# Kernel optimization log

Hardware: AMD Instinct MI355X
Metric: run time of the kernel (lower is better)

## Reference

```python
import jax, jax.numpy as jnp
import numpy as np

NUM_SEGMENTS = 50000


def _mlp(x, W1, b1, W2, b2):
    # hidden layer with ReLU, linear output (num_hidden_lyr=1)
    h = jax.nn.relu(x @ W1 + b1)
    return h @ W2 + b2


def setup_inputs() -> dict:
    key = jax.random.key(0)
    ks = jax.random.split(key, 10)
    N, D = 1000000, 128
    ins = jax.random.normal(ks[0], (N, D), dtype=jnp.float32)
    batch = jnp.sort(jax.random.randint(ks[1], (N,), 0, NUM_SEGMENTS, dtype=jnp.int64))
    s = 1.0 / np.sqrt(D)
    phi_W1 = jax.random.uniform(ks[2], (D, D), jnp.float32, -s, s)
    phi_b1 = jax.random.uniform(ks[3], (D,), jnp.float32, -s, s)
    phi_W2 = jax.random.uniform(ks[4], (D, D), jnp.float32, -s, s)
    phi_b2 = jax.random.uniform(ks[5], (D,), jnp.float32, -s, s)
    rho_W1 = jax.random.uniform(ks[6], (D, D), jnp.float32, -s, s)
    rho_b1 = jax.random.uniform(ks[7], (D,), jnp.float32, -s, s)
    rho_W2 = jax.random.uniform(ks[8], (D, D), jnp.float32, -s, s)
    rho_b2 = jax.random.uniform(ks[9], (D,), jnp.float32, -s, s)
    return {"ins": ins, "batch": batch, "dim": 0,
            "phi_W1": phi_W1, "phi_b1": phi_b1, "phi_W2": phi_W2, "phi_b2": phi_b2,
            "rho_W1": rho_W1, "rho_b1": rho_b1, "rho_W2": rho_W2, "rho_b2": rho_b2}


def reference(ins, batch, dim, phi_W1, phi_b1, phi_W2, phi_b2, rho_W1, rho_b1, rho_W2, rho_b2):
    # dim is always 0 in this usage (scatter over set elements)
    h = _mlp(ins, phi_W1, phi_b1, phi_W2, phi_b2)          # [N, out_dim]
    seg_sum = jax.ops.segment_sum(h, batch, num_segments=NUM_SEGMENTS)  # [B, out_dim]
    counts = jax.ops.segment_sum(jnp.ones((h.shape[0],), h.dtype), batch,
                                 num_segments=NUM_SEGMENTS)
    seg_mean = seg_sum / jnp.maximum(counts, 1.0)[:, None]  # scatter_mean semantics
    return _mlp(seg_mean, rho_W1, rho_b1, rho_W2, rho_b2)   # [B, out_dim]
```

## Files before the change

### kernel.cpp

```cpp
#include <hip/hip_runtime.h>
#include <hip/hip_fp16.h>

typedef _Float16 f16;
typedef __attribute__((ext_vector_type(8))) _Float16 f16x8;
typedef __attribute__((ext_vector_type(4))) _Float16 f16x4;
typedef __attribute__((ext_vector_type(4))) float f32x4;

#define NSEG 50000
#define DIM 128
#define LDST 136

#define MFMA16(a, b, c) __builtin_amdgcn_mfma_f32_16x16x32_f16((a), (b), (c), 0, 0, 0)

__global__ void zero2_kernel(float4* __restrict__ a, int n4a,
                             float4* __restrict__ b, int n4b) {
    int i = blockIdx.x * blockDim.x + threadIdx.x;
    float4 z = make_float4(0.f, 0.f, 0.f, 0.f);
    if (i < n4a) {
        a[i] = z;
    } else {
        int j = i - n4a;
        if (j < n4b) b[j] = z;
    }
}

__global__ void prepack_kernel(const float* __restrict__ w0, const float* __restrict__ w1,
                               const float* __restrict__ w2, const float* __restrict__ w3,
                               f16* __restrict__ packs) {
    int gid = blockIdx.x * blockDim.x + threadIdx.x;
    int q = gid >> 11;
    int r = gid & 2047;
    int tm = r >> 8;
    int kt = (r >> 6) & 3;
    int lane = r & 63;
    const float* W = (q == 0) ? w0 : (q == 1) ? w1 : (q == 2) ? w2 : w3;
    int mp = tm * 16 + (lane & 15);
    int kb = kt * 32 + ((lane >> 4) & 3) * 8;
    f16* dst = packs + q * 16384 + ((size_t)((tm * 4 + kt) * 64 + lane)) * 8;
#pragma unroll
    for (int j = 0; j < 8; ++j)
        dst[j] = (f16)W[(size_t)(kb + j) * DIM + mp];
}

__global__ __launch_bounds__(256, 4)
void phi_scatter_kernel(const float* __restrict__ x, const int* __restrict__ batch,
                        const f16* __restrict__ pack1, const f16* __restrict__ pack2,
                        const float* __restrict__ b1, const float* __restrict__ b2,
                        float* __restrict__ seg_sum, float* __restrict__ counts, int N) {
    __shared__ f16 buf[128 * LDST];
    __shared__ int seg_s[128];

    int tid = threadIdx.x;
    int wave = tid >> 6, lane = tid & 63, g = lane >> 4, ln = lane & 15;
    long long r0 = (long long)blockIdx.x * 128;
    int nvalid = min(128, N - (int)r0);

#pragma unroll
    for (int i = 0; i < 16; ++i) {
        int flat = i * 1024 + tid * 4;
        int row = flat >> 7, col = flat & 127;
        float4 v = make_float4(0.f, 0.f, 0.f, 0.f);
        if (row < nvalid) v = *(const float4*)(x + (r0 + row) * DIM + col);
        f16x4 h;
        h[0] = (f16)v.x; h[1] = (f16)v.y; h[2] = (f16)v.z; h[3] = (f16)v.w;
        *(f16x4*)(buf + row * LDST + col) = h;
    }
    if (tid < 128) {
        int s = 0;
        if (tid < nvalid) {
            s = batch[r0 + tid];
            s = (s < 0) ? 0 : ((s >= NSEG) ? NSEG - 1 : s);
        } else {
            s = -1;
        }
        seg_s[tid] = s;
    }
    __syncthreads();

    int tm0 = wave * 2;
    f32x4 acc[2][8];
#pragma unroll
    for (int a = 0; a < 2; ++a)
#pragma unroll
        for (int t = 0; t < 8; ++t) acc[a][t] = (f32x4){0.f, 0.f, 0.f, 0.f};

#pragma unroll
    for (int kt = 0; kt < 4; ++kt) {
        f16x8 a0 = *(const f16x8*)(pack1 + ((size_t)((tm0 + 0) * 4 + kt) * 64 + lane) * 8);
        f16x8 a1 = *(const f16x8*)(pack1 + ((size_t)((tm0 + 1) * 4 + kt) * 64 + lane) * 8);
#pragma unroll
        for (int tn = 0; tn < 8; ++tn) {
            f16x8 b = *(const f16x8*)(buf + (tn * 16 + ln) * LDST + kt * 32 + g * 8);
            acc[0][tn] = MFMA16(a0, b, acc[0][tn]);
            acc[1][tn] = MFMA16(a1, b, acc[1][tn]);
        }
    }
    __syncthreads();

#pragma unroll
    for (int a = 0; a < 2; ++a) {
        int tm = tm0 + a;
        float4 bv = *(const float4*)(b1 + tm * 16 + g * 4);
#pragma unroll
        for (int tn = 0; tn < 8; ++tn) {
            f32x4 c = acc[a][tn];
            f16x4 h;
            h[0] = (f16)fmaxf(c[0] + bv.x, 0.f);
            h[1] = (f16)fmaxf(c[1] + bv.y, 0.f);
            h[2] = (f16)fmaxf(c[2] + bv.z, 0.f);
            h[3] = (f16)fmaxf(c[3] + bv.w, 0.f);
            *(f16x4*)(buf + (tn * 16 + ln) * LDST + tm * 16 + g * 4) = h;
        }
    }
    __syncthreads();

#pragma unroll
    for (int a = 0; a < 2; ++a)
#pragma unroll
        for (int t = 0; t < 8; ++t) acc[a][t] = (f32x4){0.f, 0.f, 0.f, 0.f};
#pragma unroll
    for (int kt = 0; kt < 4; ++kt) {
        f16x8 a0 = *(const f16x8*)(pack2 + ((size_t)((tm0 + 0) * 4 + kt) * 64 + lane) * 8);
        f16x8 a1 = *(const f16x8*)(pack2 + ((size_t)((tm0 + 1) * 4 + kt) * 64 + lane) * 8);
#pragma unroll
        for (int tn = 0; tn < 8; ++tn) {
            f16x8 b = *(const f16x8*)(buf + (tn * 16 + ln) * LDST + kt * 32 + g * 8);
            acc[0][tn] = MFMA16(a0, b, acc[0][tn]);
            acc[1][tn] = MFMA16(a1, b, acc[1][tn]);
        }
    }
    __syncthreads();

#pragma unroll
    for (int a = 0; a < 2; ++a) {
        int tm = tm0 + a;
        float4 bv = *(const float4*)(b2 + tm * 16 + g * 4);
#pragma unroll
        for (int tn = 0; tn < 8; ++tn) {
            f32x4 c = acc[a][tn];
            f16x4 h;
            h[0] = (f16)(c[0] + bv.x);
            h[1] = (f16)(c[1] + bv.y);
            h[2] = (f16)(c[2] + bv.z);
            h[3] = (f16)(c[3] + bv.w);
            *(f16x4*)(buf + (tn * 16 + ln) * LDST + tm * 16 + g * 4) = h;
        }
    }
    __syncthreads();

    int n = tid & 127, half = tid >> 7;
    int m0 = half * 64;
    float accv = 0.f, cnt = 0.f;
    int cur = seg_s[m0];
#pragma unroll
    for (int grp = 0; grp < 8; ++grp) {
        float v[8];
        int s[8];
#pragma unroll
        for (int j = 0; j < 8; ++j) {
            int m = m0 + grp * 8 + j;
            s[j] = seg_s[m];
            v[j] = (float)buf[m * LDST + n];
        }
#pragma unroll
        for (int j = 0; j < 8; ++j) {
            if (s[j] != cur) {
                if (cur >= 0) {
                    atomicAdd(seg_sum + (size_t)cur * DIM + n, accv);
                    if (n == 0) atomicAdd(counts + cur, cnt);
                }
                accv = 0.f; cnt = 0.f; cur = s[j];
            }
            accv += v[j]; cnt += 1.f;
        }
    }
    if (cur >= 0) {
        atomicAdd(seg_sum + (size_t)cur * DIM + n, accv);
        if (n == 0) atomicAdd(counts + cur, cnt);
    }
}

#define RROWS 64
__global__ __launch_bounds__(256, 4)
void rho_kernel(const float* __restrict__ seg_sum, const float* __restrict__ counts,
                const f16* __restrict__ pack1, const f16* __restrict__ pack2,
                const float* __restrict__ b1, const float* __restrict__ b2,
                float* __restrict__ out) {
    __shared__ f16 buf[RROWS * LDST];

    int tid = threadIdx.x;
    int wave = tid >> 6, lane = tid & 63, g = lane >> 4, ln = lane & 15;
    int s0 = blockIdx.x * RROWS;
    int nvalid = min(RROWS, NSEG - s0);

#pragma unroll
    for (int i = 0; i < 8; ++i) {
        int flat = i * 1024 + tid * 4;
        int row = flat >> 7, col = flat & 127;
        float4 v = make_float4(0.f, 0.f, 0.f, 0.f);
        if (row < nvalid) {
            v = *(const float4*)(seg_sum + (size_t)(s0 + row) * DIM + col);
            float inv = 1.f / fmaxf(counts[s0 + row], 1.f);
            v.x *= inv; v.y *= inv; v.z *= inv; v.w *= inv;
        }
        f16x4 h;
        h[0] = (f16)v.x; h[1] = (f16)v.y; h[2] = (f16)v.z; h[3] = (f16)v.w;
        *(f16x4*)(buf + row * LDST + col) = h;
    }
    __syncthreads();

    int tm0 = wave * 2;
    f32x4 acc[2][4];
#pragma unroll
    for (int a = 0; a < 2; ++a)
#pragma unroll
        for (int t = 0; t < 4; ++t) acc[a][t] = (f32x4){0.f, 0.f, 0.f, 0.f};

#pragma unroll
    for (int kt = 0; kt < 4; ++kt) {
        f16x8 a0 = *(const f16x8*)(pack1 + ((size_t)((tm0 + 0) * 4 + kt) * 64 + lane) * 8);
        f16x8 a1 = *(const f16x8*)(pack1 + ((size_t)((tm0 + 1) * 4 + kt) * 64 + lane) * 8);
#pragma unroll
        for (int tn = 0; tn < 4; ++tn) {
            f16x8 b = *(const f16x8*)(buf + (tn * 16 + ln) * LDST + kt * 32 + g * 8);
            acc[0][tn] = MFMA16(a0, b, acc[0][tn]);
            acc[1][tn] = MFMA16(a1, b, acc[1][tn]);
        }
    }
    __syncthreads();

#pragma unroll
    for (int a = 0; a < 2; ++a) {
        int tm = tm0 + a;
        float4 bv = *(const float4*)(b1 + tm * 16 + g * 4);
#pragma unroll
        for (int tn = 0; tn < 4; ++tn) {
            f32x4 c = acc[a][tn];
            f16x4 h;
            h[0] = (f16)fmaxf(c[0] + bv.x, 0.f);
            h[1] = (f16)fmaxf(c[1] + bv.y, 0.f);
            h[2] = (f16)fmaxf(c[2] + bv.z, 0.f);
            h[3] = (f16)fmaxf(c[3] + bv.w, 0.f);
            *(f16x4*)(buf + (tn * 16 + ln) * LDST + tm * 16 + g * 4) = h;
        }
    }
    __syncthreads();

#pragma unroll
    for (int a = 0; a < 2; ++a)
#pragma unroll
        for (int t = 0; t < 4; ++t) acc[a][t] = (f32x4){0.f, 0.f, 0.f, 0.f};
#pragma unroll
    for (int kt = 0; kt < 4; ++kt) {
        f16x8 a0 = *(const f16x8*)(pack2 + ((size_t)((tm0 + 0) * 4 + kt) * 64 + lane) * 8);
        f16x8 a1 = *(const f16x8*)(pack2 + ((size_t)((tm0 + 1) * 4 + kt) * 64 + lane) * 8);
#pragma unroll
        for (int tn = 0; tn < 4; ++tn) {
            f16x8 b = *(const f16x8*)(buf + (tn * 16 + ln) * LDST + kt * 32 + g * 8);
            acc[0][tn] = MFMA16(a0, b, acc[0][tn]);
            acc[1][tn] = MFMA16(a1, b, acc[1][tn]);
        }
    }

#pragma unroll
    for (int a = 0; a < 2; ++a) {
        int tm = tm0 + a;
        float4 bv = *(const float4*)(b2 + tm * 16 + g * 4);
#pragma unroll
        for (int tn = 0; tn < 4; ++tn) {
            int srow = tn * 16 + ln;
            if (s0 + srow < NSEG) {
                f32x4 c = acc[a][tn];
                float4 o = make_float4(c[0] + bv.x, c[1] + bv.y, c[2] + bv.z, c[3] + bv.w);
                *(float4*)(out + (size_t)(s0 + srow) * DIM + tm * 16 + g * 4) = o;
            }
        }
    }
}

extern "C" void kernel_launch(void* const* d_in, const int* in_sizes, int n_in,
                              void* d_out, int out_size, void* d_ws, size_t ws_size,
                              hipStream_t stream) {
    const float* ins = (const float*)d_in[0];
    const int* batch = (const int*)d_in[1];
    const float* phi_W1 = (const float*)d_in[3];
    const float* phi_b1 = (const float*)d_in[4];
    const float* phi_W2 = (const float*)d_in[5];
    const float* phi_b2 = (const float*)d_in[6];
    const float* rho_W1 = (const float*)d_in[7];
    const float* rho_b1 = (const float*)d_in[8];
    const float* rho_W2 = (const float*)d_in[9];
    const float* rho_b2 = (const float*)d_in[10];

    int N = in_sizes[0] / DIM;

    float* seg_sum = (float*)d_out;
    char* ws = (char*)d_ws;
    float* counts = (float*)ws;
    f16*   packs  = (f16*)(ws + 200704);

    int n4a = NSEG * DIM / 4;
    int n4b = NSEG / 4;
    zero2_kernel<<<(n4a + n4b + 255) / 256, 256, 0, stream>>>((float4*)seg_sum, n4a,
                                                              (float4*)counts, n4b);

    prepack_kernel<<<32, 256, 0, stream>>>(phi_W1, phi_W2, rho_W1, rho_W2, packs);

    int nblk = (N + 127) / 128;
    phi_scatter_kernel<<<nblk, 256, 0, stream>>>(ins, batch, packs, packs + 16384,
                                                 phi_b1, phi_b2, seg_sum, counts, N);

    rho_kernel<<<(NSEG + RROWS - 1) / RROWS, 256, 0, stream>>>(seg_sum, counts,
                                                       packs + 2 * 16384, packs + 3 * 16384,
                                                       rho_b1, rho_b2, (float*)d_out);
}
```

Measured before the change: 766.2 us.

## Make phi kernel process tile chunks with register-prefetched double-buffered LDS

The phi_scatter kernel now has each block walk a chunk of 16 consecutive 128-row tiles instead of one. The next tile's x and batch values are loaded into registers while the current tile's two GEMMs and the segment scatter run, then written into a second LDS buffer. This is meant to hide global-load latency and amortise per-block setup. The cost is doubled LDS per block and a lower occupancy target (launch_bounds 2), and about 489 blocks may leave the tail unevenly spread across CUs. Separately, the zero-fill and weight-prepack kernels are merged into one launch to save a kernel launch.

```diff
diff --git a/kernel.cpp b/kernel.cpp
--- a/kernel.cpp
+++ b/kernel.cpp
@@ -9,25 +9,29 @@
 #define NSEG 50000
 #define DIM 128
 #define LDST 136
+#define CHUNK 16
 
 #define MFMA16(a, b, c) __builtin_amdgcn_mfma_f32_16x16x32_f16((a), (b), (c), 0, 0, 0)
 
-__global__ void zero2_kernel(float4* __restrict__ a, int n4a,
-                             float4* __restrict__ b, int n4b) {
-    int i = blockIdx.x * blockDim.x + threadIdx.x;
-    float4 z = make_float4(0.f, 0.f, 0.f, 0.f);
-    if (i < n4a) {
-        a[i] = z;
-    } else {
-        int j = i - n4a;
-        if (j < n4b) b[j] = z;
-    }
-}
-
-__global__ void prepack_kernel(const float* __restrict__ w0, const float* __restrict__ w1,
-                               const float* __restrict__ w2, const float* __restrict__ w3,
-                               f16* __restrict__ packs) {
-    int gid = blockIdx.x * blockDim.x + threadIdx.x;
+__global__ void setup_kernel(float4* __restrict__ za, int n4a,
+                             float4* __restrict__ zb, int n4b, int zblk,
+                             const float* __restrict__ w0, const float* __restrict__ w1,
+                             const float* __restrict__ w2, const float* __restrict__ w3,
+                             f16* __restrict__ packs) {
+    int b = blockIdx.x;
+    int tid = threadIdx.x;
+    if (b < zblk) {
+        int i = b * 256 + tid;
+        float4 z = make_float4(0.f, 0.f, 0.f, 0.f);
+        if (i < n4a) {
+            za[i] = z;
+        } else {
+            int j = i - n4a;
+            if (j < n4b) zb[j] = z;
+        }
+        return;
+    }
+    int gid = (b - zblk) * 256 + tid;
     int q = gid >> 11;
     int r = gid & 2047;
     int tm = r >> 8;
@@ -42,141 +46,178 @@
         dst[j] = (f16)W[(size_t)(kb + j) * DIM + mp];
 }
 
-__global__ __launch_bounds__(256, 4)
+__device__ __forceinline__ void stage_load(const float* __restrict__ x,
+                                           const int* __restrict__ batch,
+                                           int tile, int N, int tid,
+                                           float4 xs[16], int& sv) {
+    int r0 = tile * 128;
+    int nvalid = min(128, N - r0);
+#pragma unroll
+    for (int i = 0; i < 16; ++i) {
+        int flat = i * 1024 + tid * 4;
+        int row = flat >> 7, col = flat & 127;
+        xs[i] = make_float4(0.f, 0.f, 0.f, 0.f);
+        if (row < nvalid) xs[i] = *(const float4*)(x + (size_t)(r0 + row) * DIM + col);
+    }
+    sv = -1;
+    if (tid < 128 && tid < nvalid) {
+        int s = batch[r0 + tid];
+        sv = (s < 0) ? 0 : ((s >= NSEG) ? NSEG - 1 : s);
+    }
+}
+
+__device__ __forceinline__ void stage_write(f16* __restrict__ bufc, int* __restrict__ segc,
+                                            int tid, const float4 xs[16], int sv) {
+#pragma unroll
+    for (int i = 0; i < 16; ++i) {
+        int flat = i * 1024 + tid * 4;
+        int row = flat >> 7, col = flat & 127;
+        f16x4 h;
+        h[0] = (f16)xs[i].x; h[1] = (f16)xs[i].y; h[2] = (f16)xs[i].z; h[3] = (f16)xs[i].w;
+        *(f16x4*)(bufc + row * LDST + col) = h;
+    }
+    if (tid < 128) segc[tid] = sv;
+}
+
+__global__ __launch_bounds__(256, 2)
 void phi_scatter_kernel(const float* __restrict__ x, const int* __restrict__ batch,
                         const f16* __restrict__ pack1, const f16* __restrict__ pack2,
                         const float* __restrict__ b1, const float* __restrict__ b2,
-                        float* __restrict__ seg_sum, float* __restrict__ counts, int N) {
-    __shared__ f16 buf[128 * LDST];
-    __shared__ int seg_s[128];
+                        float* __restrict__ seg_sum, float* __restrict__ counts,
+                        int N, int ntiles) {
+    __shared__ f16 buf[2][128 * LDST];
+    __shared__ int seg_s[2][128];
 
     int tid = threadIdx.x;
     int wave = tid >> 6, lane = tid & 63, g = lane >> 4, ln = lane & 15;
-    long long r0 = (long long)blockIdx.x * 128;
-    int nvalid = min(128, N - (int)r0);
-
-#pragma unroll
-    for (int i = 0; i < 16; ++i) {
-        int flat = i * 1024 + tid * 4;
-        int row = flat >> 7, col = flat & 127;
-        float4 v = make_float4(0.f, 0.f, 0.f, 0.f);
-        if (row < nvalid) v = *(const float4*)(x + (r0 + row) * DIM + col);
-        f16x4 h;
-        h[0] = (f16)v.x; h[1] = (f16)v.y; h[2] = (f16)v.z; h[3] = (f16)v.w;
-        *(f16x4*)(buf + row * LDST + col) = h;
-    }
-    if (tid < 128) {
-        int s = 0;
-        if (tid < nvalid) {
-            s = batch[r0 + tid];
-            s = (s < 0) ? 0 : ((s >= NSEG) ? NSEG - 1 : s);
-        } else {
-            s = -1;
-        }
-        seg_s[tid] = s;
+    int tm0 = wave * 2;
+
+    int start = blockIdx.x * CHUNK;
+    int cnt_t = min(CHUNK, ntiles - start);
+    if (cnt_t <= 0) return;
+
+    {
+        float4 xs[16]; int sv;
+        stage_load(x, batch, start, N, tid, xs, sv);
+        stage_write(buf[0], seg_s[0], tid, xs, sv);
     }
     __syncthreads();
 
-    int tm0 = wave * 2;
-    f32x4 acc[2][8];
-#pragma unroll
-    for (int a = 0; a < 2; ++a)
-#pragma unroll
-        for (int t = 0; t < 8; ++t) acc[a][t] = (f32x4){0.f, 0.f, 0.f, 0.f};
-
-#pragma unroll
-    for (int kt = 0; kt < 4; ++kt) {
-        f16x8 a0 = *(const f16x8*)(pack1 + ((size_t)((tm0 + 0) * 4 + kt) * 64 + lane) * 8);
-        f16x8 a1 = *(const f16x8*)(pack1 + ((size_t)((tm0 + 1) * 4 + kt) * 64 + lane) * 8);
-#pragma unroll
-        for (int tn = 0; tn < 8; ++tn) {
-            f16x8 b = *(const f16x8*)(buf + (tn * 16 + ln) * LDST + kt * 32 + g * 8);
-            acc[0][tn] = MFMA16(a0, b, acc[0][tn]);
-            acc[1][tn] = MFMA16(a1, b, acc[1][tn]);
-        }
-    }
-    __syncthreads();
-
-#pragma unroll
-    for (int a = 0; a < 2; ++a) {
-        int tm = tm0 + a;
-        float4 bv = *(const float4*)(b1 + tm * 16 + g * 4);
-#pragma unroll
-        for (int tn = 0; tn < 8; ++tn) {
-            f32x4 c = acc[a][tn];
-            f16x4 h;
-            h[0] = (f16)fmaxf(c[0] + bv.x, 0.f);
-            h[1] = (f16)fmaxf(c[1] + bv.y, 0.f);
-            h[2] = (f16)fmaxf(c[2] + bv.z, 0.f);
-            h[3] = (f16)fmaxf(c[3] + bv.w, 0.f);
-            *(f16x4*)(buf + (tn * 16 + ln) * LDST + tm * 16 + g * 4) = h;
-        }
-    }
-    __syncthreads();
-
-#pragma unroll
-    for (int a = 0; a < 2; ++a)
-#pragma unroll
-        for (int t = 0; t < 8; ++t) acc[a][t] = (f32x4){0.f, 0.f, 0.f, 0.f};
-#pragma unroll
-    for (int kt = 0; kt < 4; ++kt) {
-        f16x8 a0 = *(const f16x8*)(pack2 + ((size_t)((tm0 + 0) * 4 + kt) * 64 + lane) * 8);
-        f16x8 a1 = *(const f16x8*)(pack2 + ((size_t)((tm0 + 1) * 4 + kt) * 64 + lane) * 8);
-#pragma unroll
-        for (int tn = 0; tn < 8; ++tn) {
-            f16x8 b = *(const f16x8*)(buf + (tn * 16 + ln) * LDST + kt * 32 + g * 8);
-            acc[0][tn] = MFMA16(a0, b, acc[0][tn]);
-            acc[1][tn] = MFMA16(a1, b, acc[1][tn]);
-        }
-    }
-    __syncthreads();
-
-#pragma unroll
-    for (int a = 0; a < 2; ++a) {
-        int tm = tm0 + a;
-        float4 bv = *(const float4*)(b2 + tm * 16 + g * 4);
-#pragma unroll
-        for (int tn = 0; tn < 8; ++tn) {
-            f32x4 c = acc[a][tn];
-            f16x4 h;
-            h[0] = (f16)(c[0] + bv.x);
-            h[1] = (f16)(c[1] + bv.y);
-            h[2] = (f16)(c[2] + bv.z);
-            h[3] = (f16)(c[3] + bv.w);
-            *(f16x4*)(buf + (tn * 16 + ln) * LDST + tm * 16 + g * 4) = h;
-        }
-    }
-    __syncthreads();
-
-    int n = tid & 127, half = tid >> 7;
-    int m0 = half * 64;
-    float accv = 0.f, cnt = 0.f;
-    int cur = seg_s[m0];
-#pragma unroll
-    for (int grp = 0; grp < 8; ++grp) {
-        float v[8];
-        int s[8];
-#pragma unroll
-        for (int j = 0; j < 8; ++j) {
-            int m = m0 + grp * 8 + j;
-            s[j] = seg_s[m];
-            v[j] = (float)buf[m * LDST + n];
-        }
-#pragma unroll
-        for (int j = 0; j < 8; ++j) {
-            if (s[j] != cur) {
-                if (cur >= 0) {
-                    atomicAdd(seg_sum + (size_t)cur * DIM + n, accv);
-                    if (n == 0) atomicAdd(counts + cur, cnt);
+    int cur = 0;
+    for (int t = 0; t < cnt_t; ++t) {
+        bool have_next = (t + 1 < cnt_t);
+        float4 xs[16]; int sv = -1;
+        if (have_next) stage_load(x, batch, start + t + 1, N, tid, xs, sv);
+
+        f16* bc = buf[cur];
+        int* sc = seg_s[cur];
+
+        f32x4 acc[2][8];
+#pragma unroll
+        for (int a = 0; a < 2; ++a)
+#pragma unroll
+            for (int tt = 0; tt < 8; ++tt) acc[a][tt] = (f32x4){0.f, 0.f, 0.f, 0.f};
+
+#pragma unroll
+        for (int kt = 0; kt < 4; ++kt) {
+            f16x8 a0 = *(const f16x8*)(pack1 + ((size_t)((tm0 + 0) * 4 + kt) * 64 + lane) * 8);
+            f16x8 a1 = *(const f16x8*)(pack1 + ((size_t)((tm0 + 1) * 4 + kt) * 64 + lane) * 8);
+#pragma unroll
+            for (int tn = 0; tn < 8; ++tn) {
+                f16x8 b = *(const f16x8*)(bc + (tn * 16 + ln) * LDST + kt * 32 + g * 8);
+                acc[0][tn] = MFMA16(a0, b, acc[0][tn]);
+                acc[1][tn] = MFMA16(a1, b, acc[1][tn]);
+            }
+        }
+        __syncthreads();
+
+#pragma unroll
+        for (int a = 0; a < 2; ++a) {
+            int tm = tm0 + a;
+            float4 bv = *(const float4*)(b1 + tm * 16 + g * 4);
+#pragma unroll
+            for (int tn = 0; tn < 8; ++tn) {
+                f32x4 c = acc[a][tn];
+                f16x4 h;
+                h[0] = (f16)fmaxf(c[0] + bv.x, 0.f);
+                h[1] = (f16)fmaxf(c[1] + bv.y, 0.f);
+                h[2] = (f16)fmaxf(c[2] + bv.z, 0.f);
+                h[3] = (f16)fmaxf(c[3] + bv.w, 0.f);
+                *(f16x4*)(bc + (tn * 16 + ln) * LDST + tm * 16 + g * 4) = h;
+            }
+        }
+        __syncthreads();
+
+#pragma unroll
+        for (int a = 0; a < 2; ++a)
+#pragma unroll
+            for (int tt = 0; tt < 8; ++tt) acc[a][tt] = (f32x4){0.f, 0.f, 0.f, 0.f};
+#pragma unroll
+        for (int kt = 0; kt < 4; ++kt) {
+            f16x8 a0 = *(const f16x8*)(pack2 + ((size_t)((tm0 + 0) * 4 + kt) * 64 + lane) * 8);
+            f16x8 a1 = *(const f16x8*)(pack2 + ((size_t)((tm0 + 1) * 4 + kt) * 64 + lane) * 8);
+#pragma unroll
+            for (int tn = 0; tn < 8; ++tn) {
+                f16x8 b = *(const f16x8*)(bc + (tn * 16 + ln) * LDST + kt * 32 + g * 8);
+                acc[0][tn] = MFMA16(a0, b, acc[0][tn]);
+                acc[1][tn] = MFMA16(a1, b, acc[1][tn]);
+            }
+        }
+        __syncthreads();
+
+#pragma unroll
+        for (int a = 0; a < 2; ++a) {
+            int tm = tm0 + a;
+            float4 bv = *(const float4*)(b2 + tm * 16 + g * 4);
+#pragma unroll
+            for (int tn = 0; tn < 8; ++tn) {
+                f32x4 c = acc[a][tn];
+                f16x4 h;
+                h[0] = (f16)(c[0] + bv.x);
+                h[1] = (f16)(c[1] + bv.y);
+                h[2] = (f16)(c[2] + bv.z);
+                h[3] = (f16)(c[3] + bv.w);
+                *(f16x4*)(bc + (tn * 16 + ln) * LDST + tm * 16 + g * 4) = h;
+            }
+        }
+        __syncthreads();
+
+        {
+            int n = tid & 127, half = tid >> 7;
+            int m0h = half * 64;
+            float accv = 0.f, cntv = 0.f;
+            int curs = sc[m0h];
+#pragma unroll
+            for (int grp = 0; grp < 8; ++grp) {
+                float v[8];
+                int s[8];
+#pragma unroll
+                for (int j = 0; j < 8; ++j) {
+                    int m = m0h + grp * 8 + j;
+                    s[j] = sc[m];
+                    v[j] = (float)bc[m * LDST + n];
                 }
-                accv = 0.f; cnt = 0.f; cur = s[j];
-            }
-            accv += v[j]; cnt += 1.f;
-        }
-    }
-    if (cur >= 0) {
-        atomicAdd(seg_sum + (size_t)cur * DIM + n, accv);
-        if (n == 0) atomicAdd(counts + cur, cnt);
+#pragma unroll
+                for (int j = 0; j < 8; ++j) {
+                    if (s[j] != curs) {
+                        if (curs >= 0) {
+                            atomicAdd(seg_sum + (size_t)curs * DIM + n, accv);
+                            if (n == 0) atomicAdd(counts + curs, cntv);
+                        }
+                        accv = 0.f; cntv = 0.f; curs = s[j];
+                    }
+                    accv += v[j]; cntv += 1.f;
+                }
+            }
+            if (curs >= 0) {
+                atomicAdd(seg_sum + (size_t)curs * DIM + n, accv);
+                if (n == 0) atomicAdd(counts + curs, cntv);
+            }
+        }
+
+        if (have_next) stage_write(buf[cur ^ 1], seg_s[cur ^ 1], tid, xs, sv);
+        __syncthreads();
+        cur ^= 1;
     }
 }
 
@@ -301,14 +342,16 @@
 
     int n4a = NSEG * DIM / 4;
     int n4b = NSEG / 4;
-    zero2_kernel<<<(n4a + n4b + 255) / 256, 256, 0, stream>>>((float4*)seg_sum, n4a,
-                                                              (float4*)counts, n4b);
-
-    prepack_kernel<<<32, 256, 0, stream>>>(phi_W1, phi_W2, rho_W1, rho_W2, packs);
-
-    int nblk = (N + 127) / 128;
+    int zblk = (n4a + n4b + 255) / 256;
+    setup_kernel<<<zblk + 32, 256, 0, stream>>>((float4*)seg_sum, n4a,
+                                                (float4*)counts, n4b, zblk,
+                                                phi_W1, phi_W2, rho_W1, rho_W2, packs);
+
+    int ntiles = (N + 127) / 128;
+    int nblk = (ntiles + CHUNK - 1) / CHUNK;
     phi_scatter_kernel<<<nblk, 256, 0, stream>>>(ins, batch, packs, packs + 16384,
-                                                 phi_b1, phi_b2, seg_sum, counts, N);
+                                                 phi_b1, phi_b2, seg_sum, counts,
+                                                 N, ntiles);
 
     rho_kernel<<<(NSEG + RROWS - 1) / RROWS, 256, 0, stream>>>(seg_sum, counts,
                                                        packs + 2 * 16384, packs + 3 * 16384,
```

After: 1.030 ms. 1.34x slower.
